# Kernel optimization log

Hardware: AMD Instinct MI355X
Metric: run time of the kernel (lower is better)

## Reference

```python
import jax, jax.numpy as jnp
import numpy as np
from jax import lax

MAX_DISP = 4  # max_displacement; kernel_size = 1


def setup_inputs() -> dict:
    key = jax.random.key(0)
    k1, k2 = jax.random.split(key)
    B, C, H, W = 8, 96, 160, 320
    in1 = jax.random.normal(k1, (B, C, H, W), dtype=jnp.float32)
    in2 = jax.random.normal(k2, (B, C, H, W), dtype=jnp.float32)
    return {"in1": in1, "in2": in2}


def reference(in1, in2):
    """FlowNet/PWC-Net correlation layer, kernel_size=1, max_displacement=4.

    out[b, w, y, x] = mean_c in1[b, c, y, x] * in2[b, c, y+dy, x+dx]
    with zero padding outside, dy = w // 9 - 4, dx = w % 9 - 4
    (matches the torch unfold window ordering).
    """
    pad = MAX_DISP
    B, C, H, W = in1.shape
    in2p = jnp.pad(in2, ((0, 0), (0, 0), (pad, pad), (pad, pad)))
    outs = []
    # fixed 9x9 displacement grid (81 slices) -- not a data-dim loop
    for dy in range(-pad, pad + 1):
        for dx in range(-pad, pad + 1):
            shifted = lax.dynamic_slice(
                in2p, (0, 0, pad + dy, pad + dx), (B, C, H, W)
            )
            outs.append(jnp.mean(in1 * shifted, axis=1))  # [B, H, W]
    return jnp.stack(outs, axis=1)  # [B, 81, H, W]
```

## Files before the change

kernel.cpp:

```cpp
#include <hip/hip_runtime.h>


#define BB 8
#define CC 96
#define HH 160
#define WW 320
#define TY 8
#define TX 32
#define CK 8
#define NCH (CC / CK)
#define HR (TY + 8)
#define SW 44
#define NT 576
#define HW (HH * WW)
#define NSLOT (CK * HR * (SW / 4))
#define NSTG 3

__global__ __launch_bounds__(NT, 2)
void corr_kernel(const float* __restrict__ in1,
                 const float* __restrict__ in2,
                 float* __restrict__ out) {
    const int x0 = blockIdx.x * TX;
    const int y0 = blockIdx.y * TY;
    const int b  = blockIdx.z;

    const int tid  = threadIdx.x;
    const int dy   = tid >> 6;
    const int lane = tid & 63;
    const int yi   = lane >> 3;
    const int xt   = lane & 7;

    __shared__ __align__(16) float s2[CK][HR][SW];

    int goff[NSTG];
    float4* lsl[NSTG];
    bool ok[NSTG];
#pragma unroll
    for (int t = 0; t < NSTG; ++t) {
        const int i = tid + t * NT;
        ok[t] = false; goff[t] = 0; lsl[t] = (float4*)&s2[0][0][0];
        if (i < NSLOT) {
            const int k = i / (HR * 11), rem = i % (HR * 11);
            const int r = rem / 11, c4 = rem % 11;
            lsl[t] = (float4*)&s2[k][r][4 * c4];
            const int yy = y0 + r - 4;
            const int xs = x0 - 4 + 4 * c4;
            if (c4 < 10 && (unsigned)yy < (unsigned)HH &&
                (unsigned)xs <= (unsigned)(WW - 4)) {
                ok[t] = true;
                goff[t] = (k * HH + yy) * WW + xs;
            }
        }
    }

    {
        const float4 z = make_float4(0.f, 0.f, 0.f, 0.f);
        float4* p = (float4*)&s2[0][0][0];
        for (int i = tid; i < NSLOT; i += NT) p[i] = z;
    }

    float acc[9][4];
#pragma unroll
    for (int i = 0; i < 9; ++i)
#pragma unroll
        for (int j = 0; j < 4; ++j) acc[i][j] = 0.0f;

    const float* in1p = in1 + ((size_t)(b * CC) * HH + y0 + yi) * WW + x0 + 4 * xt;

    const float4 z4 = make_float4(0.f, 0.f, 0.f, 0.f);
    float4 p[NSTG];
    {
        const int cb = (b * CC) * HW;
#pragma unroll
        for (int t = 0; t < NSTG; ++t)
            p[t] = ok[t] ? *(const float4*)(in2 + cb + goff[t]) : z4;
    }

    for (int ch = 0; ch < NCH; ++ch) {
        __syncthreads();
#pragma unroll
        for (int t = 0; t < NSTG; ++t)
            if (ok[t]) *lsl[t] = p[t];
        __syncthreads();

        if (ch + 1 < NCH) {
            const int cb = (b * CC + (ch + 1) * CK) * HW;
#pragma unroll
            for (int t = 0; t < NSTG; ++t)
                if (ok[t]) p[t] = *(const float4*)(in2 + cb + goff[t]);
        }

#pragma unroll
        for (int k = 0; k < CK; ++k) {
            float a[4];
            *(float4*)a = *(const float4*)(in1p + (size_t)(ch * CK + k) * HW);
            float v[12];
#pragma unroll
            for (int q = 0; q < 3; ++q)
                *(float4*)&v[4 * q] = *(const float4*)&s2[k][yi + dy][4 * xt + 4 * q];
#pragma unroll
            for (int dxi = 0; dxi < 9; ++dxi)
#pragma unroll
                for (int xi = 0; xi < 4; ++xi)
                    acc[dxi][xi] = fmaf(a[xi], v[xi + dxi], acc[dxi][xi]);
        }
    }

    const float scale = 1.0f / (float)CC;
#pragma unroll
    for (int dxi = 0; dxi < 9; ++dxi) {
        float4 o = make_float4(acc[dxi][0] * scale, acc[dxi][1] * scale,
                               acc[dxi][2] * scale, acc[dxi][3] * scale);
        float* dst = out +
            (((size_t)(b * 81 + dy * 9 + dxi) * HH + y0 + yi) * WW + x0 + 4 * xt);
        *(float4*)dst = o;
    }
}

extern "C" void kernel_launch(void* const* d_in, const int* in_sizes, int n_in,
                              void* d_out, int out_size, void* d_ws, size_t ws_size,
                              hipStream_t stream) {
    const float* in1 = (const float*)d_in[0];
    const float* in2 = (const float*)d_in[1];
    float* out = (float*)d_out;
    dim3 grid(WW / TX, HH / TY, BB);
    corr_kernel<<<grid, NT, 0, stream>>>(in1, in2, out);
}
```

Measured before the change: 317.1 us.

## Remap workgroups per XCD and batch in1 loads per channel chunk

Flattens the 3D grid to 1D and remaps block ids so each XCD handles a contiguous range of tiles. Neighbouring tiles then share that XCD's L2 for the overlapping in2 halo rows. It also issues all eight in1 float4 loads for a channel chunk up front, before the FMA loop, to increase memory-level parallelism. The cost is more live registers (32 extra floats), which could threaten the occupancy of two 576-thread blocks per CU.

```diff
diff --git a/kernel.cpp b/kernel.cpp
--- a/kernel.cpp
+++ b/kernel.cpp
@@ -15,14 +15,24 @@
 #define HW (HH * WW)
 #define NSLOT (CK * HR * (SW / 4))
 #define NSTG 3
+#define NWG (BB * (HH / TY) * (WW / TX))
+#define NXCD 8
+#define CPX (NWG / NXCD)
 
 __global__ __launch_bounds__(NT, 2)
 void corr_kernel(const float* __restrict__ in1,
                  const float* __restrict__ in2,
                  float* __restrict__ out) {
-    const int x0 = blockIdx.x * TX;
-    const int y0 = blockIdx.y * TY;
-    const int b  = blockIdx.z;
+    const int bid  = blockIdx.x;
+    const int nid  = (bid % NXCD) * CPX + bid / NXCD;
+    const int bz   = nid / ((HH / TY) * (WW / TX));
+    const int rem0 = nid % ((HH / TY) * (WW / TX));
+    const int by   = rem0 / (WW / TX);
+    const int bx   = rem0 % (WW / TX);
+
+    const int x0 = bx * TX;
+    const int y0 = by * TY;
+    const int b  = bz;
 
     const int tid  = threadIdx.x;
     const int dy   = tid >> 6;
@@ -55,8 +65,8 @@
 
     {
         const float4 z = make_float4(0.f, 0.f, 0.f, 0.f);
-        float4* p = (float4*)&s2[0][0][0];
-        for (int i = tid; i < NSLOT; i += NT) p[i] = z;
+        float4* p0 = (float4*)&s2[0][0][0];
+        for (int i = tid; i < NSLOT; i += NT) p0[i] = z;
     }
 
     float acc[9][4];
@@ -90,10 +100,13 @@
                 if (ok[t]) p[t] = *(const float4*)(in2 + cb + goff[t]);
         }
 
+        float a[CK][4];
+#pragma unroll
+        for (int k = 0; k < CK; ++k)
+            *(float4*)a[k] = *(const float4*)(in1p + (size_t)(ch * CK + k) * HW);
+
 #pragma unroll
         for (int k = 0; k < CK; ++k) {
-            float a[4];
-            *(float4*)a = *(const float4*)(in1p + (size_t)(ch * CK + k) * HW);
             float v[12];
 #pragma unroll
             for (int q = 0; q < 3; ++q)
@@ -102,7 +115,7 @@
             for (int dxi = 0; dxi < 9; ++dxi)
 #pragma unroll
                 for (int xi = 0; xi < 4; ++xi)
-                    acc[dxi][xi] = fmaf(a[xi], v[xi + dxi], acc[dxi][xi]);
+                    acc[dxi][xi] = fmaf(a[k][xi], v[xi + dxi], acc[dxi][xi]);
         }
     }
 
@@ -123,6 +136,5 @@
     const float* in1 = (const float*)d_in[0];
     const float* in2 = (const float*)d_in[1];
     float* out = (float*)d_out;
-    dim3 grid(WW / TX, HH / TY, BB);
-    corr_kernel<<<grid, NT, 0, stream>>>(in1, in2, out);
+    corr_kernel<<<dim3(NWG), dim3(NT), 0, stream>>>(in1, in2, out);
 }
```

Result: no change. 321.1 us (+1.3%).
